# Kernel optimization log

Measured on AMD Instinct MI355X. Metric: run time of the kernel, lower is better.

The kernel has to match this reference:

```python
import jax, jax.numpy as jnp
import numpy as np


def setup_inputs() -> dict:
    key = jax.random.key(0)
    k1, k2, k3, k4 = jax.random.split(key, 4)
    B, S, E, H = 8, 2048, 4096, 128  # batch, seq, embed, head_size
    scale = 1.0 / np.sqrt(E)
    return {
        "x": jax.random.normal(k1, (B, S, E), dtype=jnp.float32),
        "Wq": jax.random.normal(k2, (E, H), dtype=jnp.float32) * scale,
        "Wk": jax.random.normal(k3, (E, H), dtype=jnp.float32) * scale,
        "Wv": jax.random.normal(k4, (E, H), dtype=jnp.float32) * scale,
    }


def reference(x, Wq, Wk, Wv):
    # Single-head attention, non-flash branch, mask=None, eval-mode dropout.
    q = jnp.einsum("bse,eh->bsh", x, Wq)  # [B,S,H]
    k = jnp.einsum("bse,eh->bsh", x, Wk)
    v = jnp.einsum("bse,eh->bsh", x, Wv)
    head_size = k.shape[-1]
    scores = jnp.einsum("bqh,bkh->bqk", q, k) * (head_size ** -0.5)  # [B,S,S]
    attn = jax.nn.softmax(scores, axis=-1)
    out = jnp.einsum("bqk,bkh->bqh", attn, v)  # [B,S,H]
    return out
```

## Files before the change

### kernel.cpp

```cpp
#include <hip/hip_runtime.h>
#include <math.h>

typedef __bf16 bf16_t;
typedef bf16_t bf16x8 __attribute__((ext_vector_type(8)));
typedef float floatx4 __attribute__((ext_vector_type(4)));

#define MFMA(a, b, c) __builtin_amdgcn_mfma_f32_16x16x32_bf16(a, b, c, 0, 0, 0)

static constexpr int S = 2048, E = 4096, H = 128;

__device__ __forceinline__ void gl_lds16(const void* g, void* l) {
  __builtin_amdgcn_global_load_lds((const __attribute__((address_space(1))) void*)g,
                                   (__attribute__((address_space(3))) void*)l,
                                   16, 0, 0);
}

__global__ __launch_bounds__(256) void wt_kernel(const float* __restrict__ Wq,
                                                 const float* __restrict__ Wk,
                                                 const float* __restrict__ Wv,
                                                 bf16_t* __restrict__ Wt) {
  __shared__ bf16_t tile[64][130];
  int wb = blockIdx.x / 64;
  int eb = blockIdx.x % 64;
  const float* W = wb == 0 ? Wq : (wb == 1 ? Wk : Wv);
  int t = threadIdx.x;
  {
    int er = t >> 2, q = t & 3;
    const float4* src = (const float4*)(W + (size_t)(eb * 64 + er) * H + q * 32);
    for (int i = 0; i < 8; ++i) {
      float4 f = src[i];
      int c = q * 32 + i * 4;
      tile[er][c + 0] = (bf16_t)f.x; tile[er][c + 1] = (bf16_t)f.y;
      tile[er][c + 2] = (bf16_t)f.z; tile[er][c + 3] = (bf16_t)f.w;
    }
  }
  __syncthreads();
  {
    int h = t >> 1, half = t & 1;
    bf16_t buf[32];
    for (int j = 0; j < 32; ++j) buf[j] = tile[half * 32 + j][h];
    bf16_t* dst = Wt + (size_t)(wb * H + h) * E + eb * 64 + half * 32;
    for (int i = 0; i < 4; ++i) ((uint4*)dst)[i] = ((uint4*)buf)[i];
  }
}

__global__ __launch_bounds__(512, 2) void qkv_kernel(const float* __restrict__ X,
                                                     const bf16_t* __restrict__ Wt,
                                                     bf16_t* __restrict__ Qb,
                                                     bf16_t* __restrict__ Kb,
                                                     bf16_t* __restrict__ Vt) {
  __shared__ __align__(16) char smem[114688];
  constexpr int B0X = 0, B0W = 8192, B1X = 57344, B1W = 65536;

  int mBase = blockIdx.x * 64;
  int t = threadIdx.x, lane = t & 63, w = t >> 6;
  int r16 = lane & 15, q4 = lane >> 4;

  floatx4 acc[4][3] = {};

  int xrow = t >> 3;
  const float* xbase = X + (size_t)(mBase + xrow) * E + (t & 7) * 4;
  int wrl = lane >> 3, wg = lane & 7;

  float4 xa[2], xb[2];

#define FENCE() asm volatile("" ::: "memory")
#define WAITB(N)                                                                 \
  do {                                                                           \
    asm volatile("s_waitcnt vmcnt(" #N ") lgkmcnt(0)" ::: "memory");             \
    __builtin_amdgcn_s_barrier();                                                \
    asm volatile("" ::: "memory");                                               \
  } while (0)

#define LOAD_X(XR, K0)                                                           \
  _Pragma("unroll") for (int i = 0; i < 2; ++i)                                  \
      (XR)[i] = *(const float4*)(xbase + (K0) + i * 32);

#define STAGE_W(WOFF, K0)                                                        \
  _Pragma("unroll") for (int is = 0; is < 6; ++is) {                             \
    int row = w * 48 + is * 8 + wrl;                                             \
    int g = wg ^ (row & 7);                                                      \
    gl_lds16(Wt + (size_t)row * E + (K0) + g * 8,                                \
             smem + (WOFF) + (w * 48 + is * 8) * 128 + lane * 16);               \
  }

#define STAGE_X(XOFF, XR)                                                        \
  _Pragma("unroll") for (int i = 0; i < 2; ++i) {                                \
    float4 f = (XR)[i];                                                          \
    bf16_t pk[4] = {(bf16_t)f.x, (bf16_t)f.y, (bf16_t)f.z, (bf16_t)f.w};         \
    int gc = ((t & 7) >> 1) + i * 4;                                             \
    int g = gc ^ (xrow & 7);                                                     \
    *(uint2*)(smem + (XOFF) + xrow * 128 + g * 16 + (t & 1) * 8) = *(uint2*)pk;  \
  }

#define COMPUTE(XOFF, WOFF)                                                      \
  _Pragma("unroll") for (int kc = 0; kc < 2; ++kc) {                             \
    bf16x8 a[4], b[3];                                                           \
    _Pragma("unroll") for (int i = 0; i < 4; ++i) {                              \
      int row = i * 16 + r16;                                                    \
      int sl = (kc * 4 + q4) ^ (row & 7);                                        \
      a[i] = *(const bf16x8*)(smem + (XOFF) + row * 128 + sl * 16);              \
    }                                                                            \
    _Pragma("unroll") for (int j = 0; j < 3; ++j) {                              \
      int row = w * 48 + j * 16 + r16;                                           \
      int sl = (kc * 4 + q4) ^ (row & 7);                                        \
      b[j] = *(const bf16x8*)(smem + (WOFF) + row * 128 + sl * 16);              \
    }                                                                            \
    _Pragma("unroll") for (int i = 0; i < 4; ++i)                                \
        _Pragma("unroll") for (int j = 0; j < 3; ++j)                            \
            acc[i][j] = MFMA(a[i], b[j], acc[i][j]);                             \
  }

  LOAD_X(xa, 0);
  FENCE();
  STAGE_W(B0W, 0);
  FENCE();
  STAGE_X(B0X, xa);
  FENCE();
  LOAD_X(xb, 64);
  WAITB(2);

  for (int kb = 0; kb < 62; kb += 2) {
    STAGE_W(B1W, (kb + 1) * 64);
    FENCE();
    STAGE_X(B1X, xb);
    FENCE();
    LOAD_X(xa, (kb + 2) * 64);
    FENCE();
    COMPUTE(B0X, B0W);
    WAITB(2);

    STAGE_W(B0W, (kb + 2) * 64);
    FENCE();
    STAGE_X(B0X, xa);
    FENCE();
    LOAD_X(xb, (kb + 3) * 64);
    FENCE();
    COMPUTE(B1X, B1W);
    WAITB(2);
  }
  STAGE_W(B1W, 63 * 64);
  FENCE();
  STAGE_X(B1X, xb);
  FENCE();
  COMPUTE(B0X, B0W);
  WAITB(0);
  COMPUTE(B1X, B1W);

  int bb = mBase >> 11, sBase = mBase & 2047;
  bf16_t(*Ob)[264] = (bf16_t(*)[264])smem;
#pragma unroll
  for (int i = 0; i < 4; ++i)
#pragma unroll
    for (int j = 0; j < 3; ++j) {
      int ncol = w * 48 + j * 16;
      if (ncol >= 256) {
        int h = ncol - 256 + r16;
        bf16_t pk[4];
#pragma unroll
        for (int ii = 0; ii < 4; ++ii) pk[ii] = (bf16_t)acc[i][j][ii];
        *(uint2*)&Vt[((size_t)bb * H + h) * S + sBase + i * 16 + q4 * 4] =
            *(uint2*)pk;
      } else {
#pragma unroll
        for (int ii = 0; ii < 4; ++ii)
          Ob[i * 16 + q4 * 4 + ii][ncol + r16] = (bf16_t)acc[i][j][ii];
      }
    }
  __syncthreads();
  {
    int row = t >> 3, g = t & 7;
    bf16_t* qp = Qb + (size_t)(mBase + row) * H + g * 16;
    bf16_t* kp = Kb + (size_t)(mBase + row) * H + g * 16;
    *(uint4*)qp = *(uint4*)&Ob[row][g * 16];
    *(uint4*)(qp + 8) = *(uint4*)&Ob[row][g * 16 + 8];
    *(uint4*)kp = *(uint4*)&Ob[row][128 + g * 16];
    *(uint4*)(kp + 8) = *(uint4*)&Ob[row][128 + g * 16 + 8];
  }
#undef LOAD_X
#undef STAGE_W
#undef STAGE_X
#undef COMPUTE
#undef FENCE
#undef WAITB
}

__global__ __launch_bounds__(256, 2) void attn_kernel(const bf16_t* __restrict__ Qb,
                                                      const bf16_t* __restrict__ Kb,
                                                      const bf16_t* __restrict__ Vt,
                                                      float* __restrict__ Op,
                                                      float* __restrict__ Mp,
                                                      float* __restrict__ Lp) {
  __shared__ __align__(16) char smem[74752];

  int bid = blockIdx.x;
  int b = bid & 7, r = bid >> 3;
  int qt = r >> 1, half = r & 1;

  int t = threadIdx.x, lane = t & 63, wl = t >> 6;
  int r16 = lane & 15, q4 = lane >> 4;
  bf16_t(*Pl)[72] = (bf16_t(*)[72])(smem + 65536 + wl * 2304);

  bf16x8 qf[4];
  {
    const bf16_t* qp = Qb + (size_t)(b * S + qt * 64 + wl * 16 + r16) * H + q4 * 8;
#pragma unroll
    for (int c = 0; c < 4; ++c) qf[c] = *(const bf16x8*)(qp + c * 32);
  }
  floatx4 o[8] = {};
  float m_r[4], l_r[4];
#pragma unroll
  for (int ii = 0; ii < 4; ++ii) { m_r[ii] = -1e30f; l_r[ii] = 0.f; }
  const float scale = 0.08838834764831845f;

  int kr = lane >> 4, kg = lane & 15;
  int vr = lane >> 3, vg = lane & 7;

#define STAGE_KV(BUF, KT)                                                        \
  _Pragma("unroll") for (int is = 0; is < 4; ++is) {                             \
    int row = wl * 16 + is * 4 + kr;                                             \
    int g = kg ^ (row & 15);                                                     \
    gl_lds16(Kb + (size_t)(b * S + (KT) * 64 + row) * H + g * 8,                 \
             smem + (BUF) + (wl * 16 + is * 4) * 256 + lane * 16);               \
  }                                                                              \
  _Pragma("unroll") for (int is = 0; is < 4; ++is) {                             \
    int row = wl * 32 + is * 8 + vr;                                             \
    int g = vg ^ (row & 7);                                                      \
    gl_lds16(Vt + (size_t)(b * H + row) * S + (KT) * 64 + g * 8,                 \
             smem + (BUF) + 16384 + (wl * 32 + is * 8) * 128 + lane * 16);       \
  }

  STAGE_KV(0, half * 16);
  __syncthreads();

  for (int it = 0; it < 16; ++it) {
    int cur = (it & 1) << 15;
    if (it < 15) { STAGE_KV(cur ^ 32768, half * 16 + it + 1); }
    const char* kbase = smem + cur;
    bf16_t(*Vl)[64] = (bf16_t(*)[64])(smem + cur + 16384);

    floatx4 s4[4] = {};
#pragma unroll
    for (int c = 0; c < 4; ++c)
#pragma unroll
      for (int j = 0; j < 4; ++j) {
        int row = j * 16 + r16;
        int sl = (c * 4 + q4) ^ r16;
        bf16x8 bk = *(const bf16x8*)(kbase + row * 256 + sl * 16);
        s4[j] = MFMA(qf[c], bk, s4[j]);
      }

    float p[4][4], mx[4], ls[4], alpha[4];
#pragma unroll
    for (int ii = 0; ii < 4; ++ii) mx[ii] = -1e30f;
#pragma unroll
    for (int j = 0; j < 4; ++j)
#pragma unroll
      for (int ii = 0; ii < 4; ++ii) {
        float sv = s4[j][ii] * scale;
        p[j][ii] = sv;
        mx[ii] = fmaxf(mx[ii], sv);
      }
#pragma unroll
    for (int off = 1; off <= 8; off <<= 1)
#pragma unroll
      for (int ii = 0; ii < 4; ++ii)
        mx[ii] = fmaxf(mx[ii], __shfl_xor(mx[ii], off));
#pragma unroll
    for (int ii = 0; ii < 4; ++ii) {
      float mn = fmaxf(m_r[ii], mx[ii]);
      alpha[ii] = __expf(m_r[ii] - mn);
      m_r[ii] = mn;
      ls[ii] = 0.f;
    }
#pragma unroll
    for (int j = 0; j < 4; ++j)
#pragma unroll
      for (int ii = 0; ii < 4; ++ii) {
        float e = __expf(p[j][ii] - m_r[ii]);
        ls[ii] += e;
        Pl[q4 * 4 + ii][j * 16 + r16] = (bf16_t)e;
      }
#pragma unroll
    for (int off = 1; off <= 8; off <<= 1)
#pragma unroll
      for (int ii = 0; ii < 4; ++ii) ls[ii] += __shfl_xor(ls[ii], off);
#pragma unroll
    for (int ii = 0; ii < 4; ++ii) l_r[ii] = l_r[ii] * alpha[ii] + ls[ii];
#pragma unroll
    for (int f = 0; f < 8; ++f)
#pragma unroll
      for (int ii = 0; ii < 4; ++ii) o[f][ii] *= alpha[ii];

#pragma unroll
    for (int kc = 0; kc < 2; ++kc) {
      bf16x8 pa = *(const bf16x8*)&Pl[r16][kc * 32 + q4 * 8];
#pragma unroll
      for (int f = 0; f < 8; ++f) {
        int row = f * 16 + r16;
        int sl = (kc * 4 + q4) ^ (row & 7);
        bf16x8 bv = *(const bf16x8*)&Vl[row][sl * 8];
        o[f] = MFMA(pa, bv, o[f]);
      }
    }
    __syncthreads();
  }
#undef STAGE_KV

  int rowg = b * S + qt * 64 + wl * 16 + q4 * 4;
  float* op = Op + ((size_t)half * 16384 + rowg) * 128;
#pragma unroll
  for (int f = 0; f < 8; ++f)
#pragma unroll
    for (int ii = 0; ii < 4; ++ii)
      op[ii * 128 + f * 16 + r16] = o[f][ii];
  if (r16 == 0) {
#pragma unroll
    for (int ii = 0; ii < 4; ++ii) {
      Mp[half * 16384 + rowg + ii] = m_r[ii];
      Lp[half * 16384 + rowg + ii] = l_r[ii];
    }
  }
}

__global__ __launch_bounds__(256) void merge_kernel(const float* __restrict__ Op,
                                                    const float* __restrict__ Mp,
                                                    const float* __restrict__ Lp,
                                                    float* __restrict__ out) {
  int t = threadIdx.x;
  int row = blockIdx.x * 64 + (t >> 2);
  int c0 = (t & 3) * 32;
  float m1 = Mp[row], m2 = Mp[16384 + row];
  float l1 = Lp[row], l2 = Lp[16384 + row];
  float M = fmaxf(m1, m2);
  float e1 = __expf(m1 - M), e2 = __expf(m2 - M);
  float inv = 1.f / (e1 * l1 + e2 * l2);
  const float4* o1 = (const float4*)(Op + (size_t)row * 128 + c0);
  const float4* o2 = (const float4*)(Op + 16384ull * 128 + (size_t)row * 128 + c0);
  float4* op = (float4*)(out + (size_t)row * 128 + c0);
#pragma unroll
  for (int i = 0; i < 8; ++i) {
    float4 a = o1[i], b = o2[i];
    float4 rr;
    rr.x = (e1 * a.x + e2 * b.x) * inv;
    rr.y = (e1 * a.y + e2 * b.y) * inv;
    rr.z = (e1 * a.z + e2 * b.z) * inv;
    rr.w = (e1 * a.w + e2 * b.w) * inv;
    op[i] = rr;
  }
}

extern "C" void kernel_launch(void* const* d_in, const int* in_sizes, int n_in,
                              void* d_out, int out_size, void* d_ws, size_t ws_size,
                              hipStream_t stream) {
  const float* x = (const float*)d_in[0];
  const float* Wq = (const float*)d_in[1];
  const float* Wk = (const float*)d_in[2];
  const float* Wv = (const float*)d_in[3];
  float* out = (float*)d_out;

  bf16_t* Wt = (bf16_t*)d_ws;
  bf16_t* Qb = Wt + (size_t)384 * 4096;
  bf16_t* Kb = Qb + (size_t)16384 * 128;
  bf16_t* Vt = Kb + (size_t)16384 * 128;
  float* Op = (float*)(Vt + (size_t)8 * 128 * 2048);
  float* Mp = Op + (size_t)2 * 16384 * 128;
  float* Lp = Mp + 2 * 16384;

  wt_kernel<<<192, 256, 0, stream>>>(Wq, Wk, Wv, Wt);
  qkv_kernel<<<256, 512, 0, stream>>>(x, Wt, Qb, Kb, Vt);
  attn_kernel<<<512, 256, 0, stream>>>(Qb, Kb, Vt, Op, Mp, Lp);
  merge_kernel<<<256, 256, 0, stream>>>(Op, Mp, Lp, out);
}
```

Baseline: 459.3 us.

## Deepen X prefetch, add MFMA priority, lazy softmax rescale, MFMA row sums

In the QKV projection kernel, X register prefetch moves from one to two K-blocks ahead (odd/even registers), and MFMA sections get raised wave priority through s_setprio. In the attention kernel, the running max and the rescale of O and l are updated only when some row's new max exceeds the stored max by more than 8 (checked with a wave vote), skipping shuffles and exps in most iterations. Row sums of P come from an MFMA against a ones vector instead of shuffle reductions, and the loaded P fragments are reused across the PV MFMAs. Lazy rescaling lets exponentials grow up to e^8 before renormalisation, which costs some precision headroom, and the deeper prefetch uses more registers.

Measured after the change: 461.0 us. No clear change (+0.4%).

```diff
diff --git a/kernel.cpp b/kernel.cpp
--- a/kernel.cpp
+++ b/kernel.cpp
@@ -62,7 +62,7 @@
   const float* xbase = X + (size_t)(mBase + xrow) * E + (t & 7) * 4;
   int wrl = lane >> 3, wg = lane & 7;
 
-  float4 xa[2], xb[2];
+  float4 xo[2], xe[2];
 
 #define FENCE() asm volatile("" ::: "memory")
 #define WAITB(N)                                                                 \
@@ -94,6 +94,7 @@
   }
 
 #define COMPUTE(XOFF, WOFF)                                                      \
+  __builtin_amdgcn_s_setprio(1);                                                 \
   _Pragma("unroll") for (int kc = 0; kc < 2; ++kc) {                             \
     bf16x8 a[4], b[3];                                                           \
     _Pragma("unroll") for (int i = 0; i < 4; ++i) {                              \
@@ -109,39 +110,46 @@
     _Pragma("unroll") for (int i = 0; i < 4; ++i)                                \
         _Pragma("unroll") for (int j = 0; j < 3; ++j)                            \
             acc[i][j] = MFMA(a[i], b[j], acc[i][j]);                             \
-  }
-
-  LOAD_X(xa, 0);
+  }                                                                              \
+  __builtin_amdgcn_s_setprio(0);
+
+  LOAD_X(xe, 0);
   FENCE();
   STAGE_W(B0W, 0);
   FENCE();
-  STAGE_X(B0X, xa);
-  FENCE();
-  LOAD_X(xb, 64);
-  WAITB(2);
+  STAGE_X(B0X, xe);
+  FENCE();
+  LOAD_X(xo, 64);
+  LOAD_X(xe, 128);
+  WAITB(4);
 
   for (int kb = 0; kb < 62; kb += 2) {
     STAGE_W(B1W, (kb + 1) * 64);
     FENCE();
-    STAGE_X(B1X, xb);
-    FENCE();
-    LOAD_X(xa, (kb + 2) * 64);
+    STAGE_X(B1X, xo);
+    FENCE();
+    LOAD_X(xo, (kb + 3) * 64);
     FENCE();
     COMPUTE(B0X, B0W);
     WAITB(2);
 
     STAGE_W(B0W, (kb + 2) * 64);
     FENCE();
-    STAGE_X(B0X, xa);
-    FENCE();
-    LOAD_X(xb, (kb + 3) * 64);
-    FENCE();
-    COMPUTE(B1X, B1W);
-    WAITB(2);
+    STAGE_X(B0X, xe);
+    FENCE();
+    if (kb < 60) {
+      LOAD_X(xe, (kb + 4) * 64);
+      FENCE();
+      COMPUTE(B1X, B1W);
+      WAITB(2);
+    } else {
+      COMPUTE(B1X, B1W);
+      WAITB(0);
+    }
   }
   STAGE_W(B1W, 63 * 64);
   FENCE();
-  STAGE_X(B1X, xb);
+  STAGE_X(B1X, xo);
   FENCE();
   COMPUTE(B0X, B0W);
   WAITB(0);
@@ -207,6 +215,10 @@
 #pragma unroll
     for (int c = 0; c < 4; ++c) qf[c] = *(const bf16x8*)(qp + c * 32);
   }
+  bf16x8 onef;
+#pragma unroll
+  for (int i = 0; i < 8; ++i) onef[i] = (bf16_t)1.0f;
+
   floatx4 o[8] = {};
   float m_r[4], l_r[4];
 #pragma unroll
@@ -240,6 +252,7 @@
     bf16_t(*Vl)[64] = (bf16_t(*)[64])(smem + cur + 16384);
 
     floatx4 s4[4] = {};
+    __builtin_amdgcn_s_setprio(1);
 #pragma unroll
     for (int c = 0; c < 4; ++c)
 #pragma unroll
@@ -249,60 +262,70 @@
         bf16x8 bk = *(const bf16x8*)(kbase + row * 256 + sl * 16);
         s4[j] = MFMA(qf[c], bk, s4[j]);
       }
-
-    float p[4][4], mx[4], ls[4], alpha[4];
-#pragma unroll
-    for (int ii = 0; ii < 4; ++ii) mx[ii] = -1e30f;
+    __builtin_amdgcn_s_setprio(0);
+
+    float p[4][4], mxl[4];
+#pragma unroll
+    for (int ii = 0; ii < 4; ++ii) mxl[ii] = -1e30f;
 #pragma unroll
     for (int j = 0; j < 4; ++j)
 #pragma unroll
       for (int ii = 0; ii < 4; ++ii) {
         float sv = s4[j][ii] * scale;
         p[j][ii] = sv;
-        mx[ii] = fmaxf(mx[ii], sv);
-      }
-#pragma unroll
-    for (int off = 1; off <= 8; off <<= 1)
-#pragma unroll
-      for (int ii = 0; ii < 4; ++ii)
-        mx[ii] = fmaxf(mx[ii], __shfl_xor(mx[ii], off));
-#pragma unroll
-    for (int ii = 0; ii < 4; ++ii) {
-      float mn = fmaxf(m_r[ii], mx[ii]);
-      alpha[ii] = __expf(m_r[ii] - mn);
-      m_r[ii] = mn;
-      ls[ii] = 0.f;
+        mxl[ii] = fmaxf(mxl[ii], sv);
+      }
+    int ok = 1;
+#pragma unroll
+    for (int ii = 0; ii < 4; ++ii) ok &= (mxl[ii] <= m_r[ii] + 8.f) ? 1 : 0;
+    if (!__all(ok)) {
+      float alpha[4];
+#pragma unroll
+      for (int off = 1; off <= 8; off <<= 1)
+#pragma unroll
+        for (int ii = 0; ii < 4; ++ii)
+          mxl[ii] = fmaxf(mxl[ii], __shfl_xor(mxl[ii], off));
+#pragma unroll
+      for (int ii = 0; ii < 4; ++ii) {
+        float mn = fmaxf(m_r[ii], mxl[ii]);
+        alpha[ii] = __expf(m_r[ii] - mn);
+        m_r[ii] = mn;
+        l_r[ii] *= alpha[ii];
+      }
+#pragma unroll
+      for (int f = 0; f < 8; ++f)
+#pragma unroll
+        for (int ii = 0; ii < 4; ++ii) o[f][ii] *= alpha[ii];
     }
 #pragma unroll
     for (int j = 0; j < 4; ++j)
 #pragma unroll
       for (int ii = 0; ii < 4; ++ii) {
         float e = __expf(p[j][ii] - m_r[ii]);
-        ls[ii] += e;
         Pl[q4 * 4 + ii][j * 16 + r16] = (bf16_t)e;
       }
-#pragma unroll
-    for (int off = 1; off <= 8; off <<= 1)
-#pragma unroll
-      for (int ii = 0; ii < 4; ++ii) ls[ii] += __shfl_xor(ls[ii], off);
-#pragma unroll
-    for (int ii = 0; ii < 4; ++ii) l_r[ii] = l_r[ii] * alpha[ii] + ls[ii];
-#pragma unroll
-    for (int f = 0; f < 8; ++f)
-#pragma unroll
-      for (int ii = 0; ii < 4; ++ii) o[f][ii] *= alpha[ii];
-
-#pragma unroll
-    for (int kc = 0; kc < 2; ++kc) {
-      bf16x8 pa = *(const bf16x8*)&Pl[r16][kc * 32 + q4 * 8];
-#pragma unroll
-      for (int f = 0; f < 8; ++f) {
-        int row = f * 16 + r16;
-        int sl = (kc * 4 + q4) ^ (row & 7);
-        bf16x8 bv = *(const bf16x8*)&Vl[row][sl * 8];
-        o[f] = MFMA(pa, bv, o[f]);
-      }
-    }
+
+    bf16x8 pa0 = *(const bf16x8*)&Pl[r16][q4 * 8];
+    bf16x8 pa1 = *(const bf16x8*)&Pl[r16][32 + q4 * 8];
+    __builtin_amdgcn_s_setprio(1);
+    floatx4 lsv = {};
+    lsv = MFMA(pa0, onef, lsv);
+    lsv = MFMA(pa1, onef, lsv);
+#pragma unroll
+    for (int f = 0; f < 8; ++f) {
+      int row = f * 16 + r16;
+      int sl = q4 ^ (row & 7);
+      o[f] = MFMA(pa0, *(const bf16x8*)&Vl[row][sl * 8], o[f]);
+    }
+#pragma unroll
+    for (int f = 0; f < 8; ++f) {
+      int row = f * 16 + r16;
+      int sl = (4 + q4) ^ (row & 7);
+      o[f] = MFMA(pa1, *(const bf16x8*)&Vl[row][sl * 8], o[f]);
+    }
+    __builtin_amdgcn_s_setprio(0);
+#pragma unroll
+    for (int ii = 0; ii < 4; ++ii) l_r[ii] += lsv[ii];
     __syncthreads();
   }
 #undef STAGE_KV
```
